# Kernel optimization log

Hardware: AMD Instinct MI355X
Metric: run time of the kernel (lower is better)

The kernel has to match this reference:

```python
import jax, jax.numpy as jnp
import numpy as np

EPS = 1e-7  # K.epsilon()


def setup_inputs() -> dict:
    key = jax.random.key(0)
    k1, k2, k3 = jax.random.split(key, 3)
    B, T, D = 32, 2048, 1024
    one = jax.random.normal(k1, (B, D), dtype=jnp.float32)
    many = jax.random.normal(k2, (B, T, D), dtype=jnp.float32)
    W = jax.random.normal(k3, (D, D), dtype=jnp.float32) * (1.0 / np.sqrt(D))
    return {"one": one, "many": many, "W": W}


def reference(one, many, W):
    # logits = batch_dot(tanh(many @ W), one, axes=[2,1]) -> [B, T]
    proj = jnp.tanh(jnp.einsum('btd,de->bte', many, W))       # [B,T,D]
    logits = jnp.einsum('btd,bd->bt', proj, one)               # [B,T]
    # stable softmax with Keras epsilon in denominator
    ai = jnp.exp(logits - jnp.max(logits, axis=-1, keepdims=True))
    att_weights = ai / (jnp.sum(ai, axis=-1, keepdims=True) + EPS)  # [B,T]
    result = jnp.einsum('btd,bt->bd', many, att_weights)       # [B,D]
    return result, att_weights
```

## Files before the change

### kernel.cpp

```cpp
#include <hip/hip_runtime.h>
#include <hip/hip_bf16.h>

typedef _Float16 half8v __attribute__((ext_vector_type(8)));
typedef __fp16  fp16x2 __attribute__((ext_vector_type(2)));
typedef float floatx4 __attribute__((ext_vector_type(4)));

#define NB 32
#define NT 2048
#define ND 1024
#define NM (NB * NT)

#define GL16(g, l)                                                             \
    __builtin_amdgcn_global_load_lds(                                          \
        (const __attribute__((address_space(1))) void*)(g),                    \
        (__attribute__((address_space(3))) void*)(l), 16, 0, 0)

__device__ __forceinline__ float fast_tanh(float x) {
    x = fminf(9.0f, fmaxf(-9.0f, x));
    float e = __builtin_amdgcn_exp2f(x * 2.8853900817779268f);
    return (e - 1.0f) * __builtin_amdgcn_rcpf(e + 1.0f);
}

__global__ __launch_bounds__(256)
void wt_kernel(const float* __restrict__ W, _Float16* __restrict__ Wt) {
    __shared__ float tile[32][33];
    int tx = threadIdx.x, ty = threadIdx.y;
    int bx = blockIdx.x, by = blockIdx.y;
    #pragma unroll
    for (int i = 0; i < 4; ++i) {
        int y = by * 32 + ty + i * 8;
        tile[ty + i * 8][tx] = W[y * ND + bx * 32 + tx];
    }
    __syncthreads();
    #pragma unroll
    for (int i = 0; i < 4; ++i) {
        int e = bx * 32 + ty + i * 8;
        Wt[e * ND + by * 32 + tx] = (_Float16)tile[tx][ty + i * 8];
    }
}

__global__ __launch_bounds__(256)
void conv_kernel(const float* __restrict__ many, _Float16* __restrict__ manyh) {
    size_t idx = ((size_t)blockIdx.x * 256 + threadIdx.x) * 8;
    size_t stride = (size_t)gridDim.x * 256 * 8;
    for (size_t i = idx; i < (size_t)NM * ND; i += stride) {
        float4 a = *reinterpret_cast<const float4*>(many + i);
        float4 b = *reinterpret_cast<const float4*>(many + i + 4);
        union { _Float16 h[8]; uint4 u; } o;
        o.h[0] = (_Float16)a.x; o.h[1] = (_Float16)a.y;
        o.h[2] = (_Float16)a.z; o.h[3] = (_Float16)a.w;
        o.h[4] = (_Float16)b.x; o.h[5] = (_Float16)b.y;
        o.h[6] = (_Float16)b.z; o.h[7] = (_Float16)b.w;
        *reinterpret_cast<uint4*>(manyh + i) = o.u;
    }
}

__global__ __launch_bounds__(256, 2)
void gemm_logits_h(const _Float16* __restrict__ manyh, const _Float16* __restrict__ Wt,
                   const float* __restrict__ one, float* __restrict__ logits) {
    __shared__ uint4 LDSQ[4096];
    char* Ld = (char*)LDSQ;

    int bid = blockIdx.x;
    int j = (bid & 7) * 512 + (bid >> 3);
    int mb = j >> 3, nb = j & 7;
    int m0 = mb * 128, n0 = nb * 128;

    int tid = threadIdx.x;
    int lane = tid & 63, w = tid >> 6;
    int wr = w >> 1, wc = w & 1;
    int l15 = lane & 15, l4 = lane >> 4;

    const char* aS = (const char*)manyh + ((size_t)(m0 + (tid >> 3)) << 11)
                   + (size_t)(((tid & 7) ^ ((tid >> 3) & 7)) << 4);
    const char* bS = (const char*)Wt + ((size_t)(n0 + (tid >> 3)) << 11)
                   + (size_t)(((tid & 7) ^ ((tid >> 3) & 7)) << 4);

    floatx4 acc[4][4] = {};

#define STAGE(KB, BUFOFF) do {                                                 \
    int kby_ = (KB) * 2;                                                       \
    _Pragma("unroll")                                                          \
    for (int i_ = 0; i_ < 4; ++i_)                                             \
        GL16(aS + kby_ + i_ * 65536, Ld + (BUFOFF) + tid * 16 + i_ * 4096);    \
    _Pragma("unroll")                                                          \
    for (int i_ = 0; i_ < 4; ++i_)                                             \
        GL16(bS + kby_ + i_ * 65536,                                           \
             Ld + (BUFOFF) + 16384 + tid * 16 + i_ * 4096);                    \
} while (0)

#define COMPUTE(BUFOFF) do {                                                   \
    _Pragma("unroll")                                                          \
    for (int ks = 0; ks < 64; ks += 32) {                                      \
        half8v af[4], bf[4];                                                   \
        _Pragma("unroll")                                                      \
        for (int mi = 0; mi < 4; ++mi) {                                       \
            int r_ = wr * 64 + mi * 16 + l15;                                  \
            int c_ = (ks >> 3) + l4;                                           \
            af[mi] = *(const half8v*)(Ld + (BUFOFF) + r_ * 128                 \
                                      + ((c_ ^ (r_ & 7)) << 4));               \
        }                                                                      \
        _Pragma("unroll")                                                      \
        for (int ni = 0; ni < 4; ++ni) {                                       \
            int r_ = wc * 64 + ni * 16 + l15;                                  \
            int c_ = (ks >> 3) + l4;                                           \
            bf[ni] = *(const half8v*)(Ld + (BUFOFF) + 16384 + r_ * 128         \
                                      + ((c_ ^ (r_ & 7)) << 4));               \
        }                                                                      \
        _Pragma("unroll")                                                      \
        for (int mi = 0; mi < 4; ++mi)                                         \
            _Pragma("unroll")                                                  \
            for (int ni = 0; ni < 4; ++ni)                                     \
                acc[mi][ni] = __builtin_amdgcn_mfma_f32_16x16x32_f16(          \
                    af[mi], bf[ni], acc[mi][ni], 0, 0, 0);                     \
    }                                                                          \
} while (0)

    STAGE(0, 0);
    __syncthreads();
    #pragma unroll 1
    for (int t = 0; t < 16; t += 2) {
        STAGE((t + 1) << 6, 32768);
        COMPUTE(0);
        __syncthreads();
        if (t < 14) STAGE((t + 2) << 6, 0);
        COMPUTE(32768);
        __syncthreads();
    }
#undef STAGE
#undef COMPUTE

    int bidx = m0 >> 11;
    float onev[4];
    #pragma unroll
    for (int ni = 0; ni < 4; ++ni)
        onev[ni] = one[(bidx << 10) + n0 + wc * 64 + ni * 16 + l15];

    #pragma unroll
    for (int mi = 0; mi < 4; ++mi) {
        float part[4] = {0.f, 0.f, 0.f, 0.f};
        #pragma unroll
        for (int ni = 0; ni < 4; ++ni)
            #pragma unroll
            for (int b = 0; b < 4; ++b)
                part[b] += fast_tanh(acc[mi][ni][b]) * onev[ni];
        #pragma unroll
        for (int off = 1; off < 16; off <<= 1)
            #pragma unroll
            for (int b = 0; b < 4; ++b)
                part[b] += __shfl_xor(part[b], off, 64);
        #pragma unroll
        for (int b = 0; b < 4; ++b)
            if (l15 == mi * 4 + b)
                atomicAdd(&logits[m0 + wr * 64 + mi * 16 + l4 * 4 + b], part[b]);
    }
}

__global__ __launch_bounds__(256, 2)
void gemm_logits(const float* __restrict__ many, const _Float16* __restrict__ Wt,
                 const float* __restrict__ one, float* __restrict__ logits) {
    __shared__ uint4 AsQ[2048];
    __shared__ uint4 BsQ[1024];
    char* AsB = (char*)AsQ;
    char* BsB = (char*)BsQ;

    int bid = blockIdx.x;
    int j = (bid & 7) * 512 + (bid >> 3);
    int mb = j >> 3, nb = j & 7;
    int m0 = mb * 128, n0 = nb * 128;

    int tid = threadIdx.x;
    int lane = tid & 63, w = tid >> 6;
    int wr = w >> 1, wc = w & 1;
    int l15 = lane & 15, l4 = lane >> 4;

    const char* aS = (const char*)many + ((size_t)(m0 + (tid >> 4)) << 12)
        + (size_t)(((tid & 15) ^ ((tid >> 4) & 7)) << 4);
    const char* bS = (const char*)Wt + ((size_t)(n0 + (tid >> 3)) << 11)
        + (size_t)(((tid & 7) ^ ((tid >> 3) & 7)) << 4);
    char* aD = AsB + tid * 16;
    char* bD = BsB + tid * 16;

    floatx4 acc[4][4] = {};

    for (int kb = 0; kb < 1024; kb += 64) {
        #pragma unroll
        for (int i = 0; i < 8; ++i)
            GL16(aS + kb * 4 + i * 65536, aD + i * 4096);
        #pragma unroll
        for (int i = 0; i < 4; ++i)
            GL16(bS + kb * 2 + i * 65536, bD + i * 4096);
        __syncthreads();

        #pragma unroll
        for (int ks = 0; ks < 64; ks += 32) {
            half8v af[4], bf[4];
            #pragma unroll
            for (int mi = 0; mi < 4; ++mi) {
                int r = wr * 64 + mi * 16 + l15;
                int s = l15 & 7;
                const char* base = AsB + r * 256;
                int c0 = (ks >> 2) + l4 * 2;
                float4 x = *(const float4*)(base + (size_t)((c0 ^ s) << 4));
                float4 y = *(const float4*)(base + (size_t)(((c0 + 1) ^ s) << 4));
                union { fp16x2 p[4]; half8v h; } u;
                u.p[0] = __builtin_amdgcn_cvt_pkrtz(x.x, x.y);
                u.p[1] = __builtin_amdgcn_cvt_pkrtz(x.z, x.w);
                u.p[2] = __builtin_amdgcn_cvt_pkrtz(y.x, y.y);
                u.p[3] = __builtin_amdgcn_cvt_pkrtz(y.z, y.w);
                af[mi] = u.h;
            }
            #pragma unroll
            for (int ni = 0; ni < 4; ++ni) {
                int r = wc * 64 + ni * 16 + l15;
                int s = l15 & 7;
                int c = (ks >> 3) + l4;
                bf[ni] = *(const half8v*)(BsB + r * 128 + (size_t)((c ^ s) << 4));
            }
            #pragma unroll
            for (int mi = 0; mi < 4; ++mi)
                #pragma unroll
                for (int ni = 0; ni < 4; ++ni)
                    acc[mi][ni] = __builtin_amdgcn_mfma_f32_16x16x32_f16(
                        af[mi], bf[ni], acc[mi][ni], 0, 0, 0);
        }
        __syncthreads();
    }

    int bidx = m0 >> 11;
    float onev[4];
    #pragma unroll
    for (int ni = 0; ni < 4; ++ni)
        onev[ni] = one[(bidx << 10) + n0 + wc * 64 + ni * 16 + l15];

    #pragma unroll
    for (int mi = 0; mi < 4; ++mi) {
        float part[4] = {0.f, 0.f, 0.f, 0.f};
        #pragma unroll
        for (int ni = 0; ni < 4; ++ni)
            #pragma unroll
            for (int b = 0; b < 4; ++b)
                part[b] += fast_tanh(acc[mi][ni][b]) * onev[ni];
        #pragma unroll
        for (int off = 1; off < 16; off <<= 1)
            #pragma unroll
            for (int b = 0; b < 4; ++b)
                part[b] += __shfl_xor(part[b], off, 64);
        #pragma unroll
        for (int b = 0; b < 4; ++b)
            if (l15 == mi * 4 + b)
                atomicAdd(&logits[m0 + wr * 64 + mi * 16 + l4 * 4 + b], part[b]);
    }
}

__global__ __launch_bounds__(256)
void softmax_kernel(const float* __restrict__ logits, float* __restrict__ att) {
    int b = blockIdx.x, tid = threadIdx.x;
    const float* lr = logits + (b << 11);
    float lv[8];
    float mx = -1e30f;
    #pragma unroll
    for (int i = 0; i < 8; ++i) { lv[i] = lr[tid + (i << 8)]; mx = fmaxf(mx, lv[i]); }
    #pragma unroll
    for (int off = 1; off < 64; off <<= 1) mx = fmaxf(mx, __shfl_xor(mx, off, 64));
    __shared__ float redm[4];
    __shared__ float reds[4];
    int wv = tid >> 6;
    if ((tid & 63) == 0) redm[wv] = mx;
    __syncthreads();
    mx = fmaxf(fmaxf(redm[0], redm[1]), fmaxf(redm[2], redm[3]));
    float s = 0.f;
    #pragma unroll
    for (int i = 0; i < 8; ++i) { lv[i] = expf(lv[i] - mx); s += lv[i]; }
    #pragma unroll
    for (int off = 1; off < 64; off <<= 1) s += __shfl_xor(s, off, 64);
    if ((tid & 63) == 0) reds[wv] = s;
    __syncthreads();
    s = reds[0] + reds[1] + reds[2] + reds[3];
    float inv = 1.0f / (s + 1e-7f);
    #pragma unroll
    for (int i = 0; i < 8; ++i) att[(b << 11) + tid + (i << 8)] = lv[i] * inv;
}

__global__ __launch_bounds__(256)
void out_kernel_h(const _Float16* __restrict__ manyh, const float* __restrict__ att,
                  float* __restrict__ out) {
    int b = blockIdx.x >> 4, tch = blockIdx.x & 15;
    int tid = threadIdx.x;
    __shared__ float aw[128];
    if (tid < 128) aw[tid] = att[(b << 11) + tch * 128 + tid];
    __syncthreads();
    const _Float16* mp = manyh + (((size_t)b * NT + tch * 128) << 10) + tid * 4;
    float a0 = 0.f, a1 = 0.f, a2 = 0.f, a3 = 0.f;
    for (int t = 0; t < 128; ++t) {
        float wgt = aw[t];
        union { _Float16 h[4]; uint2 u; } v;
        v.u = *reinterpret_cast<const uint2*>(mp + ((size_t)t << 10));
        a0 = fmaf((float)v.h[0], wgt, a0); a1 = fmaf((float)v.h[1], wgt, a1);
        a2 = fmaf((float)v.h[2], wgt, a2); a3 = fmaf((float)v.h[3], wgt, a3);
    }
    float* op = out + (b << 10) + tid * 4;
    atomicAdd(op + 0, a0); atomicAdd(op + 1, a1);
    atomicAdd(op + 2, a2); atomicAdd(op + 3, a3);
}

__global__ __launch_bounds__(256)
void out_kernel(const float* __restrict__ many, const float* __restrict__ att,
                float* __restrict__ out) {
    int b = blockIdx.x >> 4, tch = blockIdx.x & 15;
    int tid = threadIdx.x;
    __shared__ float aw[128];
    if (tid < 128) aw[tid] = att[(b << 11) + tch * 128 + tid];
    __syncthreads();
    const float* mp = many + (((size_t)b * NT + tch * 128) << 10) + tid * 4;
    float ax = 0.f, ay = 0.f, az = 0.f, aww = 0.f;
    for (int t = 0; t < 128; ++t) {
        float wgt = aw[t];
        float4 v = *reinterpret_cast<const float4*>(mp + ((size_t)t << 10));
        ax = fmaf(v.x, wgt, ax); ay = fmaf(v.y, wgt, ay);
        az = fmaf(v.z, wgt, az); aww = fmaf(v.w, wgt, aww);
    }
    float* op = out + (b << 10) + tid * 4;
    atomicAdd(op + 0, ax); atomicAdd(op + 1, ay);
    atomicAdd(op + 2, az); atomicAdd(op + 3, aww);
}

extern "C" void kernel_launch(void* const* d_in, const int* in_sizes, int n_in,
                              void* d_out, int out_size, void* d_ws, size_t ws_size,
                              hipStream_t stream) {
    const float* one  = (const float*)d_in[0];
    const float* many = (const float*)d_in[1];
    const float* W    = (const float*)d_in[2];
    float* out = (float*)d_out;

    size_t wtB = (size_t)ND * ND * 2;
    size_t lgB = (size_t)NM * 4;
    size_t mhB = (size_t)NM * ND * 2;
    _Float16* Wt    = (_Float16*)d_ws;
    float*    logits = (float*)((char*)d_ws + wtB);
    _Float16* manyh = (_Float16*)((char*)d_ws + wtB + lgB);
    float*    att   = out + NB * ND;
    bool big = ws_size >= wtB + lgB + mhB;

    (void)hipMemsetAsync(out, 0, (size_t)NB * ND * sizeof(float), stream);
    (void)hipMemsetAsync(logits, 0, (size_t)NM * sizeof(float), stream);

    wt_kernel<<<dim3(32, 32), dim3(32, 8), 0, stream>>>(W, Wt);
    if (big) {
        conv_kernel<<<2048, 256, 0, stream>>>(many, manyh);
        gemm_logits_h<<<4096, 256, 0, stream>>>(manyh, Wt, one, logits);
    } else {
        gemm_logits<<<4096, 256, 0, stream>>>(many, Wt, one, logits);
    }
    softmax_kernel<<<NB, 256, 0, stream>>>(logits, att);
    if (big) out_kernel_h<<<NB * 16, 256, 0, stream>>>(manyh, att, out);
    else     out_kernel<<<NB * 16, 256, 0, stream>>>(many, att, out);
}
```

Measured before the change: 260.5 us.

## Replace fp16 logits GEMM with 256x256-tile, 8-wave, 4-stage pipelined kernel

Rewrites the fp16 logits GEMM to use 256x256 output tiles with 512 threads (8 waves), a 4-deep ring of 32-wide K slices loaded via global_load_lds, and fine-grained vmcnt waits instead of full __syncthreads double-buffering. Each wave computes 128x64 in two halves, interleaving the next-stage loads with MFMA bursts and using s_setprio to favor math. The larger tile raises arithmetic intensity and halves atomic traffic per output, at the cost of more registers and 128KB LDS per block, which may limit occupancy.

```diff
diff --git a/kernel.cpp b/kernel.cpp
--- a/kernel.cpp
+++ b/kernel.cpp
@@ -55,80 +55,90 @@
     }
 }
 
-__global__ __launch_bounds__(256, 2)
-void gemm_logits_h(const _Float16* __restrict__ manyh, const _Float16* __restrict__ Wt,
-                   const float* __restrict__ one, float* __restrict__ logits) {
-    __shared__ uint4 LDSQ[4096];
+__global__ __launch_bounds__(512, 2)
+void gemm_logits_8p(const _Float16* __restrict__ manyh, const _Float16* __restrict__ Wt,
+                    const float* __restrict__ one, float* __restrict__ logits) {
+    __shared__ uint4 LDSQ[8192];
     char* Ld = (char*)LDSQ;
 
     int bid = blockIdx.x;
-    int j = (bid & 7) * 512 + (bid >> 3);
-    int mb = j >> 3, nb = j & 7;
-    int m0 = mb * 128, n0 = nb * 128;
+    int j = (bid & 7) * 128 + (bid >> 3);
+    int mb = j >> 2, nb = j & 3;
+    int m0 = mb * 256, n0 = nb * 256;
 
     int tid = threadIdx.x;
     int lane = tid & 63, w = tid >> 6;
-    int wr = w >> 1, wc = w & 1;
+    int wr = w >> 2, wc = w & 3;
     int l15 = lane & 15, l4 = lane >> 4;
 
-    const char* aS = (const char*)manyh + ((size_t)(m0 + (tid >> 3)) << 11)
-                   + (size_t)(((tid & 7) ^ ((tid >> 3) & 7)) << 4);
-    const char* bS = (const char*)Wt + ((size_t)(n0 + (tid >> 3)) << 11)
-                   + (size_t)(((tid & 7) ^ ((tid >> 3) & 7)) << 4);
-
-    floatx4 acc[4][4] = {};
-
-#define STAGE(KB, BUFOFF) do {                                                 \
-    int kby_ = (KB) * 2;                                                       \
-    _Pragma("unroll")                                                          \
-    for (int i_ = 0; i_ < 4; ++i_)                                             \
-        GL16(aS + kby_ + i_ * 65536, Ld + (BUFOFF) + tid * 16 + i_ * 4096);    \
-    _Pragma("unroll")                                                          \
-    for (int i_ = 0; i_ < 4; ++i_)                                             \
-        GL16(bS + kby_ + i_ * 65536,                                           \
-             Ld + (BUFOFF) + 16384 + tid * 16 + i_ * 4096);                    \
-} while (0)
-
-#define COMPUTE(BUFOFF) do {                                                   \
-    _Pragma("unroll")                                                          \
-    for (int ks = 0; ks < 64; ks += 32) {                                      \
-        half8v af[4], bf[4];                                                   \
-        _Pragma("unroll")                                                      \
-        for (int mi = 0; mi < 4; ++mi) {                                       \
-            int r_ = wr * 64 + mi * 16 + l15;                                  \
-            int c_ = (ks >> 3) + l4;                                           \
-            af[mi] = *(const half8v*)(Ld + (BUFOFF) + r_ * 128                 \
-                                      + ((c_ ^ (r_ & 7)) << 4));               \
-        }                                                                      \
-        _Pragma("unroll")                                                      \
-        for (int ni = 0; ni < 4; ++ni) {                                       \
-            int r_ = wc * 64 + ni * 16 + l15;                                  \
-            int c_ = (ks >> 3) + l4;                                           \
-            bf[ni] = *(const half8v*)(Ld + (BUFOFF) + 16384 + r_ * 128         \
-                                      + ((c_ ^ (r_ & 7)) << 4));               \
-        }                                                                      \
-        _Pragma("unroll")                                                      \
-        for (int mi = 0; mi < 4; ++mi)                                         \
-            _Pragma("unroll")                                                  \
-            for (int ni = 0; ni < 4; ++ni)                                     \
-                acc[mi][ni] = __builtin_amdgcn_mfma_f32_16x16x32_f16(          \
-                    af[mi], bf[ni], acc[mi][ni], 0, 0, 0);                     \
-    }                                                                          \
-} while (0)
-
-    STAGE(0, 0);
-    __syncthreads();
+    const char* aS = (const char*)manyh + ((size_t)(m0 + (tid >> 2)) << 11)
+                   + (size_t)(((tid & 3) ^ ((tid >> 3) & 3)) << 4);
+    const char* bS = (const char*)Wt   + ((size_t)(n0 + (tid >> 2)) << 11)
+                   + (size_t)(((tid & 3) ^ ((tid >> 3) & 3)) << 4);
+
+#define STAGE2(QBASE, TP) do {                                                 \
+        int nxt_ = ((TP) & 3) * 32768;                                         \
+        int kn_ = (TP) * 64;                                                   \
+        const char* s_ = (QBASE) < 2 ? aS : bS;                                \
+        GL16(s_ + kn_,          Ld + nxt_ + (QBASE) * 8192 + tid * 16);        \
+        GL16(s_ + 262144 + kn_, Ld + nxt_ + (QBASE) * 8192 + 8192 + tid * 16); \
+    } while (0)
+
+    floatx4 acc[8][4] = {};
+
+    #pragma unroll
+    for (int pre = 0; pre < 3; ++pre) { STAGE2(0, pre); STAGE2(2, pre); }
+    asm volatile("s_waitcnt vmcnt(8)" ::: "memory");
+    __builtin_amdgcn_sched_barrier(0);
+    __builtin_amdgcn_s_barrier();
+
     #pragma unroll 1
-    for (int t = 0; t < 16; t += 2) {
-        STAGE((t + 1) << 6, 32768);
-        COMPUTE(0);
-        __syncthreads();
-        if (t < 14) STAGE((t + 2) << 6, 0);
-        COMPUTE(32768);
-        __syncthreads();
-    }
-#undef STAGE
-#undef COMPUTE
+    for (int t = 0; t < 32; ++t) {
+        int cur = (t & 3) * 32768;
+        half8v af[4], bf[4];
+        #pragma unroll
+        for (int mi = 0; mi < 4; ++mi) {
+            int r = wr * 128 + mi * 16 + l15;
+            af[mi] = *(const half8v*)(Ld + cur + r * 64 + ((l4 ^ ((r >> 1) & 3)) << 4));
+        }
+        #pragma unroll
+        for (int ni = 0; ni < 4; ++ni) {
+            int r = wc * 64 + ni * 16 + l15;
+            bf[ni] = *(const half8v*)(Ld + cur + 16384 + r * 64 + ((l4 ^ ((r >> 1) & 3)) << 4));
+        }
+        if (t < 29) STAGE2(0, t + 3);
+        __builtin_amdgcn_s_barrier();
+        __builtin_amdgcn_s_setprio(1);
+        #pragma unroll
+        for (int mi = 0; mi < 4; ++mi)
+            #pragma unroll
+            for (int ni = 0; ni < 4; ++ni)
+                acc[mi][ni] = __builtin_amdgcn_mfma_f32_16x16x32_f16(
+                    af[mi], bf[ni], acc[mi][ni], 0, 0, 0);
+        __builtin_amdgcn_s_setprio(0);
+        __builtin_amdgcn_s_barrier();
+        #pragma unroll
+        for (int mi = 0; mi < 4; ++mi) {
+            int r = wr * 128 + 64 + mi * 16 + l15;
+            af[mi] = *(const half8v*)(Ld + cur + r * 64 + ((l4 ^ ((r >> 1) & 3)) << 4));
+        }
+        if (t < 29) STAGE2(2, t + 3);
+        __builtin_amdgcn_s_barrier();
+        __builtin_amdgcn_s_setprio(1);
+        #pragma unroll
+        for (int mi = 0; mi < 4; ++mi)
+            #pragma unroll
+            for (int ni = 0; ni < 4; ++ni)
+                acc[4 + mi][ni] = __builtin_amdgcn_mfma_f32_16x16x32_f16(
+                    af[mi], bf[ni], acc[4 + mi][ni], 0, 0, 0);
+        __builtin_amdgcn_s_setprio(0);
+        if (t <= 28)      asm volatile("s_waitcnt vmcnt(8)" ::: "memory");
+        else if (t == 29) asm volatile("s_waitcnt vmcnt(4)" ::: "memory");
+        else if (t == 30) asm volatile("s_waitcnt vmcnt(0)" ::: "memory");
+        __builtin_amdgcn_sched_barrier(0);
+        __builtin_amdgcn_s_barrier();
+    }
+#undef STAGE2
 
     int bidx = m0 >> 11;
     float onev[4];
@@ -137,7 +147,7 @@
         onev[ni] = one[(bidx << 10) + n0 + wc * 64 + ni * 16 + l15];
 
     #pragma unroll
-    for (int mi = 0; mi < 4; ++mi) {
+    for (int mi = 0; mi < 8; ++mi) {
         float part[4] = {0.f, 0.f, 0.f, 0.f};
         #pragma unroll
         for (int ni = 0; ni < 4; ++ni)
@@ -151,8 +161,8 @@
                 part[b] += __shfl_xor(part[b], off, 64);
         #pragma unroll
         for (int b = 0; b < 4; ++b)
-            if (l15 == mi * 4 + b)
-                atomicAdd(&logits[m0 + wr * 64 + mi * 16 + l4 * 4 + b], part[b]);
+            if (l15 == ((mi * 4 + b) & 15))
+                atomicAdd(&logits[m0 + wr * 128 + mi * 16 + l4 * 4 + b], part[b]);
     }
 }
 
@@ -348,7 +358,7 @@
     wt_kernel<<<dim3(32, 32), dim3(32, 8), 0, stream>>>(W, Wt);
     if (big) {
         conv_kernel<<<2048, 256, 0, stream>>>(many, manyh);
-        gemm_logits_h<<<4096, 256, 0, stream>>>(manyh, Wt, one, logits);
+        gemm_logits_8p<<<1024, 512, 0, stream>>>(manyh, Wt, one, logits);
     } else {
         gemm_logits<<<4096, 256, 0, stream>>>(many, Wt, one, logits);
     }
```

Measured after the change: 279.5 us. 7.3% more time.
